# Kernel optimization log

Measured on AMD Instinct MI355X. Metric: run time of the kernel, lower is better.

## Reference

```python
import jax, jax.numpy as jnp
import numpy as np

BN_EPS = 1e-5
TAU = 1.0

def _conv(x, w, pad, groups=1):
    return jax.lax.conv_general_dilated(
        x, w, (1, 1), [(pad, pad), (pad, pad)],
        feature_group_count=groups,
        dimension_numbers=('NCHW', 'OIHW', 'NCHW'))

def _bn(x, p):
    # p: (4, C) rows = gamma, beta, running_mean, running_var (eval-mode BN)
    g, b, m, v = p[0], p[1], p[2], p[3]
    scale = g * jax.lax.rsqrt(v + BN_EPS)
    shift = b - m * scale
    return x * scale[None, :, None, None] + shift[None, :, None, None]

def _dsconv(x, dw, bn1, pw, bn2, pad):
    c = x.shape[1]
    h = jax.nn.silu(_bn(_conv(x, dw, pad, groups=c), bn1))
    return jax.nn.silu(_bn(_conv(h, pw, 0), bn2))

def _make_bn(key, ch):
    k1, k2, k3, k4 = jax.random.split(key, 4)
    g = 1.0 + 0.1 * jax.random.normal(k1, (ch,), jnp.float32)
    b = 0.1 * jax.random.normal(k2, (ch,), jnp.float32)
    m = 0.1 * jax.random.normal(k3, (ch,), jnp.float32)
    v = 0.5 + jax.random.uniform(k4, (ch,), jnp.float32)
    return jnp.stack([g, b, m, v])

def setup_inputs() -> dict:
    key = jax.random.key(0)
    ks = jax.random.split(key, 18)
    B, C, H, W = 4, 256, 128, 128
    P, K = 64, 8
    inp = {
        'x':      jax.random.normal(ks[0], (B, C, H, W), jnp.float32),
        'fp_w1':  0.05 * jax.random.normal(ks[1], (P, C, 1, 1), jnp.float32),
        'fp_bn1': _make_bn(ks[2], P),
        'fp_dw':  0.2 * jax.random.normal(ks[3], (P, 1, 3, 3), jnp.float32),
        'fp_bn2': _make_bn(ks[4], P),
        'protos': jax.random.normal(ks[5], (K, P), jnp.float32),
        'bs_dw':  0.2 * jax.random.normal(ks[6], (1, 1, 3, 3), jnp.float32),
        'bs_bn1': _make_bn(ks[7], 1),
        'bs_pw':  0.2 * jax.random.normal(ks[8], (8, 1, 1, 1), jnp.float32),
        'bs_bn2': _make_bn(ks[9], 8),
        'bl_dw':  0.2 * jax.random.normal(ks[10], (1, 1, 5, 5), jnp.float32),
        'bl_bn1': _make_bn(ks[11], 1),
        'bl_pw':  0.2 * jax.random.normal(ks[12], (8, 1, 1, 1), jnp.float32),
        'bl_bn2': _make_bn(ks[13], 8),
        'fuse_w': 0.2 * jax.random.normal(ks[14], (1, 16, 1, 1), jnp.float32),
        'fuse_b': 0.1 * jax.random.normal(ks[15], (1,), jnp.float32),
        'gamma':  0.5 * jax.random.normal(ks[16], (1,), jnp.float32),
    }
    return inp

def reference(x, fp_w1, fp_bn1, fp_dw, fp_bn2, protos,
              bs_dw, bs_bn1, bs_pw, bs_bn2,
              bl_dw, bl_bn1, bl_pw, bl_bn2,
              fuse_w, fuse_b, gamma):
    # feature_proj: 1x1 conv -> BN -> SiLU -> depthwise 3x3 -> BN -> SiLU
    h = jax.nn.silu(_bn(_conv(x, fp_w1, 0), fp_bn1))
    proj = jax.nn.silu(_bn(_conv(h, fp_dw, 1, groups=fp_dw.shape[0]), fp_bn2))

    # deviation: min L2 distance to K bg prototypes, per-image min-max normalized
    B, P, H, W = proj.shape
    feat = proj.reshape(B, P, H * W).transpose(0, 2, 1)      # (B, HW, P)
    d2 = ((feat * feat).sum(-1, keepdims=True)               # (B, HW, 1)
          + (protos * protos).sum(-1)                        # (K,)
          - 2.0 * jnp.einsum('bnp,kp->bnk', feat, protos))   # (B, HW, K)
    dist = jnp.sqrt(jnp.maximum(d2, 0.0))
    min_dist = dist.min(axis=2) / (TAU + 1e-6)               # (B, HW)
    d_min = min_dist.min(axis=1, keepdims=True)
    d_max = min_dist.max(axis=1, keepdims=True)
    deviation = ((min_dist - d_min) / (d_max - d_min + 1e-6)).reshape(B, 1, H, W)

    # deviation -> attention head: two DS-conv branches (3x3 and 5x5), fuse 1x1, sigmoid
    f1 = _dsconv(deviation, bs_dw, bs_bn1, bs_pw, bs_bn2, pad=1)
    f2 = _dsconv(deviation, bl_dw, bl_bn1, bl_pw, bl_bn2, pad=2)
    attn = jax.nn.sigmoid(_conv(jnp.concatenate([f1, f2], axis=1), fuse_w, 0)
                          + fuse_b[None, :, None, None])
    return x + gamma * (x * attn)
```

## Files before the change

### kernel.cpp

```cpp
#include <hip/hip_runtime.h>
#include <math.h>

#define C_IN 256
#define P_CH 64
#define H_IMG 128
#define W_IMG 128
#define HW (H_IMG*W_IMG)
#define N_IMG 4
#define K_PROTO 8
#define BN_EPS 1e-5f

#define OFF_WT     0
#define OFF_BIASA  16384
#define OFF_PNORM  16448
#define OFF_MINMAX 16456
#define OFF_H      16464
#define OFF_MD     (16464 + 4194304)
#define OFF_ATTN   (OFF_MD + 65536)

__device__ __forceinline__ float silu_f(float x) { return x / (1.f + __expf(-x)); }

__global__ void prep_kernel(const float* __restrict__ w1, const float* __restrict__ bn1,
                            const float* __restrict__ protos, float* __restrict__ ws)
{
    int bx = blockIdx.x, tid = threadIdx.x;
    if (bx < 64) {
        int idx = bx * 256 + tid;
        int c = idx >> 6, p = idx & 63;
        float sc = bn1[p] * rsqrtf(bn1[192 + p] + BN_EPS);
        ws[OFF_WT + idx] = w1[p * C_IN + c] * sc;
    } else {
        if (tid < 64) {
            float sc = bn1[tid] * rsqrtf(bn1[192 + tid] + BN_EPS);
            ws[OFF_BIASA + tid] = bn1[64 + tid] - bn1[128 + tid] * sc;
        }
        if (tid < 8) {
            float s = 0.f;
            for (int p = 0; p < 64; ++p) { float v = protos[tid * 64 + p]; s += v * v; }
            ws[OFF_PNORM + tid] = s;
        }
        if (tid < 4) {
            unsigned* mm = (unsigned*)(ws + OFF_MINMAX);
            mm[tid * 2]     = 0x7f7fffffu;
            mm[tid * 2 + 1] = 0u;
        }
    }
}

__global__ __launch_bounds__(256, 2) void conv1x1_kernel(
    const float* __restrict__ x, const float* __restrict__ wt,
    const float* __restrict__ bias, float* __restrict__ h)
{
    __shared__ float xs[2][8][128];
    int bx = blockIdx.x;
    int img = bx >> 7;
    int row = bx & 127;
    int tid = threadIdx.x;
    int pgrp = tid >> 6;
    int lane = tid & 63;
    int sc_ = tid >> 5;
    int sp_ = (tid & 31) * 4;

    const float* xbase = x + (size_t)img * C_IN * HW + row * W_IMG;
    float* hb = h + (size_t)img * P_CH * HW + row * W_IMG;

    float a0[16], a1[16];
#pragma unroll
    for (int j = 0; j < 16; ++j) { a0[j] = 0.f; a1[j] = 0.f; }

    {
        float4 f0 = *(const float4*)(xbase + (size_t)sc_ * HW + sp_);
        *(float4*)&xs[0][sc_][sp_] = f0;
    }
    __syncthreads();

    for (int k = 0; k < 32; ++k) {
        float4 nxt;
        if (k < 31)
            nxt = *(const float4*)(xbase + (size_t)((k + 1) * 8 + sc_) * HW + sp_);

        const float (*xb)[128] = xs[k & 1];
        int c0 = k * 8;
#pragma unroll
        for (int cl = 0; cl < 8; ++cl) {
            float xv0 = xb[cl][lane];
            float xv1 = xb[cl][lane + 64];
            int wof = __builtin_amdgcn_readfirstlane((c0 + cl) * 64 + pgrp * 16);
            const float* w = wt + wof;
#pragma unroll
            for (int j = 0; j < 16; ++j) {
                a0[j] = fmaf(xv0, w[j], a0[j]);
                a1[j] = fmaf(xv1, w[j], a1[j]);
            }
        }
        if (k < 31)
            *(float4*)&xs[(k + 1) & 1][sc_][sp_] = nxt;
        __syncthreads();
    }

    int bof = __builtin_amdgcn_readfirstlane(pgrp * 16);
#pragma unroll
    for (int j = 0; j < 16; ++j) {
        int p = bof + j;
        float bb = bias[p];
        hb[(size_t)p * HW + lane]      = silu_f(a0[j] + bb);
        hb[(size_t)p * HW + lane + 64] = silu_f(a1[j] + bb);
    }
}

__global__ __launch_bounds__(256) void dwconv_dev_kernel(
    const float* __restrict__ h, const float* __restrict__ dw,
    const float* __restrict__ bn2, const float* __restrict__ protos,
    const float* __restrict__ pnorm, float* __restrict__ md,
    unsigned* __restrict__ minmax)
{
    __shared__ float tile[2][8 * 324];
    __shared__ float red[512];
    int img = blockIdx.x >> 6;
    int t = blockIdx.x & 63;
    int y0 = (t >> 3) << 4, x0 = (t & 7) << 4;
    int tid = threadIdx.x;
    int ty = tid >> 4, tx = tid & 15;

    const float* himg = h + (size_t)img * P_CH * HW;

    int  pre_off[11];
    bool pre_ok[11];
    bool pre_v[11];
#pragma unroll
    for (int r = 0; r < 11; ++r) {
        int l = tid + r * 256;
        bool valid = l < 2592;
        int cl = l / 324;
        int rr = l - cl * 324;
        int ly = rr / 18, lx = rr - ly * 18;
        int yy = y0 - 1 + ly, xx = x0 - 1 + lx;
        bool inb = (yy >= 0) & (yy < H_IMG) & (xx >= 0) & (xx < W_IMG);
        pre_v[r] = valid;
        pre_ok[r] = valid && inb;
        pre_off[r] = cl * HW + (inb ? (yy * W_IMG + xx) : 0);
    }

    float norm2 = 0.f;
    float dot[K_PROTO];
#pragma unroll
    for (int k = 0; k < K_PROTO; ++k) dot[k] = 0.f;

    {
#pragma unroll
        for (int r = 0; r < 11; ++r) {
            float v = pre_ok[r] ? himg[pre_off[r]] : 0.f;
            if (pre_v[r]) tile[0][tid + r * 256] = v;
        }
    }
    __syncthreads();

    for (int k = 0; k < 8; ++k) {
        float pf[11];
        if (k < 7) {
            const float* hs = himg + (size_t)(k + 1) * 8 * HW;
#pragma unroll
            for (int r = 0; r < 11; ++r)
                pf[r] = pre_ok[r] ? hs[pre_off[r]] : 0.f;
        }

        const float* tb = tile[k & 1];
        int c0 = k * 8;
#pragma unroll
        for (int cl = 0; cl < 8; ++cl) {
            int ch = c0 + cl;
            const float* tc = tb + cl * 324;
            const float* wch = dw + ch * 9;
            float s = 0.f;
#pragma unroll
            for (int dy = 0; dy < 3; ++dy)
#pragma unroll
                for (int dx = 0; dx < 3; ++dx)
                    s = fmaf(tc[(ty + dy) * 18 + tx + dx], wch[dy * 3 + dx], s);
            float g = bn2[ch], bb = bn2[64 + ch], m = bn2[128 + ch], vv = bn2[192 + ch];
            float scale = g * rsqrtf(vv + BN_EPS);
            float val = silu_f(scale * s + (bb - m * scale));
            norm2 = fmaf(val, val, norm2);
#pragma unroll
            for (int kk = 0; kk < K_PROTO; ++kk)
                dot[kk] = fmaf(val, protos[kk * 64 + ch], dot[kk]);
        }

        if (k < 7) {
            float* tn = tile[(k + 1) & 1];
#pragma unroll
            for (int r = 0; r < 11; ++r)
                if (pre_v[r]) tn[tid + r * 256] = pf[r];
        }
        __syncthreads();
    }

    float d2min = 1e30f;
#pragma unroll
    for (int k = 0; k < K_PROTO; ++k)
        d2min = fminf(d2min, norm2 + pnorm[k] - 2.f * dot[k]);
    float mdv = sqrtf(fmaxf(d2min, 0.f)) * (1.f / 1.000001f);
    md[img * HW + (y0 + ty) * W_IMG + (x0 + tx)] = mdv;

    red[tid] = mdv; red[256 + tid] = mdv;
    __syncthreads();
    for (int s2 = 128; s2 > 0; s2 >>= 1) {
        if (tid < s2) {
            red[tid]       = fminf(red[tid], red[tid + s2]);
            red[256 + tid] = fmaxf(red[256 + tid], red[256 + tid + s2]);
        }
        __syncthreads();
    }
    if (tid == 0) {
        atomicMin(&minmax[img * 2],     __float_as_uint(red[0]));
        atomicMax(&minmax[img * 2 + 1], __float_as_uint(red[256]));
    }
}

__global__ __launch_bounds__(256) void attn_kernel(
    const float* __restrict__ md, const unsigned* __restrict__ minmax,
    const float* __restrict__ bs_dw, const float* __restrict__ bs_bn1,
    const float* __restrict__ bs_pw, const float* __restrict__ bs_bn2,
    const float* __restrict__ bl_dw, const float* __restrict__ bl_bn1,
    const float* __restrict__ bl_pw, const float* __restrict__ bl_bn2,
    const float* __restrict__ fuse_w, const float* __restrict__ fuse_b,
    float* __restrict__ attn)
{
    __shared__ float tile[20 * 20];
    int img = blockIdx.x >> 6;
    int t = blockIdx.x & 63;
    int y0 = (t >> 3) << 4, x0 = (t & 7) << 4;
    int tid = threadIdx.x;
    int ty = tid >> 4, tx = tid & 15;

    float fdmin = __uint_as_float(minmax[img * 2]);
    float fdmax = __uint_as_float(minmax[img * 2 + 1]);
    float inv = 1.f / (fdmax - fdmin + 1e-6f);

    const float* mdi = md + img * HW;
    for (int l = tid; l < 400; l += 256) {
        int ly = l / 20, lx = l - ly * 20;
        int yy = y0 - 2 + ly, xx = x0 - 2 + lx;
        float v = 0.f;
        if (yy >= 0 && yy < H_IMG && xx >= 0 && xx < W_IMG)
            v = (mdi[yy * W_IMG + xx] - fdmin) * inv;
        tile[l] = v;
    }
    __syncthreads();

    float c3 = 0.f;
#pragma unroll
    for (int dy = 0; dy < 3; ++dy)
#pragma unroll
        for (int dx = 0; dx < 3; ++dx)
            c3 = fmaf(tile[(ty + 1 + dy) * 20 + tx + 1 + dx], bs_dw[dy * 3 + dx], c3);
    float c5 = 0.f;
#pragma unroll
    for (int dy = 0; dy < 5; ++dy)
#pragma unroll
        for (int dx = 0; dx < 5; ++dx)
            c5 = fmaf(tile[(ty + dy) * 20 + tx + dx], bl_dw[dy * 5 + dx], c5);

    float s1 = bs_bn1[0] * rsqrtf(bs_bn1[3] + BN_EPS);
    float t1 = silu_f(s1 * c3 + (bs_bn1[1] - bs_bn1[2] * s1));
    float s2 = bl_bn1[0] * rsqrtf(bl_bn1[3] + BN_EPS);
    float t2 = silu_f(s2 * c5 + (bl_bn1[1] - bl_bn1[2] * s2));

    float acc = fuse_b[0];
#pragma unroll
    for (int c = 0; c < 8; ++c) {
        float scs = bs_bn2[c] * rsqrtf(bs_bn2[24 + c] + BN_EPS);
        float u1 = silu_f(scs * (bs_pw[c] * t1) + (bs_bn2[8 + c] - bs_bn2[16 + c] * scs));
        acc = fmaf(fuse_w[c], u1, acc);
        float scl = bl_bn2[c] * rsqrtf(bl_bn2[24 + c] + BN_EPS);
        float u2 = silu_f(scl * (bl_pw[c] * t2) + (bl_bn2[8 + c] - bl_bn2[16 + c] * scl));
        acc = fmaf(fuse_w[8 + c], u2, acc);
    }
    float a = 1.f / (1.f + __expf(-acc));
    attn[img * HW + (y0 + ty) * W_IMG + (x0 + tx)] = a;
}

__global__ __launch_bounds__(256) void final_kernel(
    const float* __restrict__ x, const float* __restrict__ attn,
    const float* __restrict__ gamma, float* __restrict__ out)
{
    size_t i = ((size_t)blockIdx.x * 256 + (size_t)threadIdx.x) * 4;
    float g = gamma[0];
    int b = (int)(i / ((size_t)C_IN * HW));
    int hw = (int)(i % HW);
    const float4 xv = *(const float4*)(x + i);
    const float4 av = *(const float4*)(attn + (size_t)b * HW + hw);
    float4 o;
    o.x = xv.x * (1.f + g * av.x);
    o.y = xv.y * (1.f + g * av.y);
    o.z = xv.z * (1.f + g * av.z);
    o.w = xv.w * (1.f + g * av.w);
    *(float4*)(out + i) = o;
}

extern "C" void kernel_launch(void* const* d_in, const int* in_sizes, int n_in,
                              void* d_out, int out_size, void* d_ws, size_t ws_size,
                              hipStream_t stream) {
    const float* x      = (const float*)d_in[0];
    const float* fp_w1  = (const float*)d_in[1];
    const float* fp_bn1 = (const float*)d_in[2];
    const float* fp_dw  = (const float*)d_in[3];
    const float* fp_bn2 = (const float*)d_in[4];
    const float* protos = (const float*)d_in[5];
    const float* bs_dw  = (const float*)d_in[6];
    const float* bs_bn1 = (const float*)d_in[7];
    const float* bs_pw  = (const float*)d_in[8];
    const float* bs_bn2 = (const float*)d_in[9];
    const float* bl_dw  = (const float*)d_in[10];
    const float* bl_bn1 = (const float*)d_in[11];
    const float* bl_pw  = (const float*)d_in[12];
    const float* bl_bn2 = (const float*)d_in[13];
    const float* fuse_w = (const float*)d_in[14];
    const float* fuse_b = (const float*)d_in[15];
    const float* gamma  = (const float*)d_in[16];
    float* ws  = (float*)d_ws;
    float* out = (float*)d_out;

    prep_kernel<<<65, 256, 0, stream>>>(fp_w1, fp_bn1, protos, ws);
    conv1x1_kernel<<<512, 256, 0, stream>>>(x, ws + OFF_WT, ws + OFF_BIASA, ws + OFF_H);
    dwconv_dev_kernel<<<256, 256, 0, stream>>>(ws + OFF_H, fp_dw, fp_bn2, protos,
                                               ws + OFF_PNORM, ws + OFF_MD,
                                               (unsigned*)(ws + OFF_MINMAX));
    attn_kernel<<<256, 256, 0, stream>>>(ws + OFF_MD, (const unsigned*)(ws + OFF_MINMAX),
                                         bs_dw, bs_bn1, bs_pw, bs_bn2,
                                         bl_dw, bl_bn1, bl_pw, bl_bn2,
                                         fuse_w, fuse_b, ws + OFF_ATTN);
    final_kernel<<<16384, 256, 0, stream>>>(x, ws + OFF_ATTN, gamma, out);
}
```

Baseline: 225.2 us.

## Split conv1x1 rows into halves and split dwconv channels across four thread groups

The 1x1 conv kernel now processes half-rows (64 pixels) per block, doubling the grid to 1024 blocks with fewer accumulators per thread and a higher occupancy bound. The depthwise/deviation kernel uses 1024-thread blocks where four 256-thread groups each handle 16 channels. Partial norms and dot products are combined through shared memory, and the min/max reduction now uses wavefront shuffles. The aim is more parallelism on a 256-CU GPU, where the old grids underfilled the device. The cost is re-reading weights per half-row and extra shared-memory reduction and syncs.

```diff
diff --git a/kernel.cpp b/kernel.cpp
--- a/kernel.cpp
+++ b/kernel.cpp
@@ -47,53 +47,50 @@
     }
 }
 
-__global__ __launch_bounds__(256, 2) void conv1x1_kernel(
+__global__ __launch_bounds__(256, 4) void conv1x1_kernel(
     const float* __restrict__ x, const float* __restrict__ wt,
     const float* __restrict__ bias, float* __restrict__ h)
 {
-    __shared__ float xs[2][8][128];
+    __shared__ float xs[2][8][64];
     int bx = blockIdx.x;
-    int img = bx >> 7;
-    int row = bx & 127;
+    int img = bx >> 8;
+    int rem = bx & 255;
+    int row = rem >> 1;
+    int half = rem & 1;
     int tid = threadIdx.x;
     int pgrp = tid >> 6;
     int lane = tid & 63;
-    int sc_ = tid >> 5;
-    int sp_ = (tid & 31) * 4;
-
-    const float* xbase = x + (size_t)img * C_IN * HW + row * W_IMG;
-    float* hb = h + (size_t)img * P_CH * HW + row * W_IMG;
-
-    float a0[16], a1[16];
-#pragma unroll
-    for (int j = 0; j < 16; ++j) { a0[j] = 0.f; a1[j] = 0.f; }
-
-    {
-        float4 f0 = *(const float4*)(xbase + (size_t)sc_ * HW + sp_);
-        *(float4*)&xs[0][sc_][sp_] = f0;
-    }
+    int sc_ = tid >> 4;
+    int sp_ = (tid & 15) * 4;
+
+    const float* xbase = x + (size_t)img * C_IN * HW + row * W_IMG + half * 64;
+    float* hb = h + (size_t)img * P_CH * HW + row * W_IMG + half * 64;
+
+    float acc[16];
+#pragma unroll
+    for (int j = 0; j < 16; ++j) acc[j] = 0.f;
+
+    if (tid < 128)
+        *(float4*)&xs[0][sc_][sp_] = *(const float4*)(xbase + (size_t)sc_ * HW + sp_);
     __syncthreads();
 
     for (int k = 0; k < 32; ++k) {
         float4 nxt;
-        if (k < 31)
+        if (k < 31 && tid < 128)
             nxt = *(const float4*)(xbase + (size_t)((k + 1) * 8 + sc_) * HW + sp_);
 
-        const float (*xb)[128] = xs[k & 1];
+        const float (*xb)[64] = xs[k & 1];
         int c0 = k * 8;
 #pragma unroll
         for (int cl = 0; cl < 8; ++cl) {
-            float xv0 = xb[cl][lane];
-            float xv1 = xb[cl][lane + 64];
+            float xv = xb[cl][lane];
             int wof = __builtin_amdgcn_readfirstlane((c0 + cl) * 64 + pgrp * 16);
             const float* w = wt + wof;
 #pragma unroll
-            for (int j = 0; j < 16; ++j) {
-                a0[j] = fmaf(xv0, w[j], a0[j]);
-                a1[j] = fmaf(xv1, w[j], a1[j]);
-            }
-        }
-        if (k < 31)
+            for (int j = 0; j < 16; ++j)
+                acc[j] = fmaf(xv, w[j], acc[j]);
+        }
+        if (k < 31 && tid < 128)
             *(float4*)&xs[(k + 1) & 1][sc_][sp_] = nxt;
         __syncthreads();
     }
@@ -102,34 +99,34 @@
 #pragma unroll
     for (int j = 0; j < 16; ++j) {
         int p = bof + j;
-        float bb = bias[p];
-        hb[(size_t)p * HW + lane]      = silu_f(a0[j] + bb);
-        hb[(size_t)p * HW + lane + 64] = silu_f(a1[j] + bb);
-    }
-}
-
-__global__ __launch_bounds__(256) void dwconv_dev_kernel(
+        hb[(size_t)p * HW + lane] = silu_f(acc[j] + bias[p]);
+    }
+}
+
+__global__ __launch_bounds__(1024) void dwconv_dev_kernel(
     const float* __restrict__ h, const float* __restrict__ dw,
     const float* __restrict__ bn2, const float* __restrict__ protos,
     const float* __restrict__ pnorm, float* __restrict__ md,
     unsigned* __restrict__ minmax)
 {
-    __shared__ float tile[2][8 * 324];
-    __shared__ float red[512];
+    __shared__ float smem[4 * 8 * 324];
     int img = blockIdx.x >> 6;
     int t = blockIdx.x & 63;
     int y0 = (t >> 3) << 4, x0 = (t & 7) << 4;
     int tid = threadIdx.x;
-    int ty = tid >> 4, tx = tid & 15;
+    int q = tid >> 8;
+    int qtid = tid & 255;
+    int ty = qtid >> 4, tx = qtid & 15;
 
     const float* himg = h + (size_t)img * P_CH * HW;
+    float* qt = smem + q * (8 * 324);
 
     int  pre_off[11];
     bool pre_ok[11];
     bool pre_v[11];
 #pragma unroll
     for (int r = 0; r < 11; ++r) {
-        int l = tid + r * 256;
+        int l = qtid + r * 256;
         bool valid = l < 2592;
         int cl = l / 324;
         int rr = l - cl * 324;
@@ -147,29 +144,29 @@
     for (int k = 0; k < K_PROTO; ++k) dot[k] = 0.f;
 
     {
+        const float* hs = himg + (size_t)(q * 16) * HW;
 #pragma unroll
         for (int r = 0; r < 11; ++r) {
-            float v = pre_ok[r] ? himg[pre_off[r]] : 0.f;
-            if (pre_v[r]) tile[0][tid + r * 256] = v;
-        }
-    }
-    __syncthreads();
-
-    for (int k = 0; k < 8; ++k) {
+            float v = pre_ok[r] ? hs[pre_off[r]] : 0.f;
+            if (pre_v[r]) qt[qtid + r * 256] = v;
+        }
+    }
+    __syncthreads();
+
+    for (int k = 0; k < 2; ++k) {
         float pf[11];
-        if (k < 7) {
-            const float* hs = himg + (size_t)(k + 1) * 8 * HW;
+        if (k == 0) {
+            const float* hs = himg + (size_t)(q * 16 + 8) * HW;
 #pragma unroll
             for (int r = 0; r < 11; ++r)
                 pf[r] = pre_ok[r] ? hs[pre_off[r]] : 0.f;
         }
 
-        const float* tb = tile[k & 1];
-        int c0 = k * 8;
+        int c0 = q * 16 + k * 8;
 #pragma unroll
         for (int cl = 0; cl < 8; ++cl) {
             int ch = c0 + cl;
-            const float* tc = tb + cl * 324;
+            const float* tc = qt + cl * 324;
             const float* wch = dw + ch * 9;
             float s = 0.f;
 #pragma unroll
@@ -186,34 +183,62 @@
                 dot[kk] = fmaf(val, protos[kk * 64 + ch], dot[kk]);
         }
 
-        if (k < 7) {
-            float* tn = tile[(k + 1) & 1];
+        if (k == 0) {
+            __syncthreads();
 #pragma unroll
             for (int r = 0; r < 11; ++r)
-                if (pre_v[r]) tn[tid + r * 256] = pf[r];
-        }
-        __syncthreads();
-    }
-
-    float d2min = 1e30f;
-#pragma unroll
-    for (int k = 0; k < K_PROTO; ++k)
-        d2min = fminf(d2min, norm2 + pnorm[k] - 2.f * dot[k]);
-    float mdv = sqrtf(fmaxf(d2min, 0.f)) * (1.f / 1.000001f);
-    md[img * HW + (y0 + ty) * W_IMG + (x0 + tx)] = mdv;
-
-    red[tid] = mdv; red[256 + tid] = mdv;
-    __syncthreads();
-    for (int s2 = 128; s2 > 0; s2 >>= 1) {
-        if (tid < s2) {
-            red[tid]       = fminf(red[tid], red[tid + s2]);
-            red[256 + tid] = fmaxf(red[256 + tid], red[256 + tid + s2]);
-        }
-        __syncthreads();
-    }
+                if (pre_v[r]) qt[qtid + r * 256] = pf[r];
+            __syncthreads();
+        }
+    }
+    __syncthreads();
+
+    float* P = smem;
+    {
+        float* dst = P + (q * 256 + qtid) * 9;
+        dst[0] = norm2;
+#pragma unroll
+        for (int kk = 0; kk < K_PROTO; ++kk) dst[1 + kk] = dot[kk];
+    }
+    __syncthreads();
+
+    float wmin = 1e30f, wmax = -1e30f, mdv = 0.f;
+    if (q == 0) {
+        float n2 = 0.f, dd[K_PROTO];
+#pragma unroll
+        for (int kk = 0; kk < K_PROTO; ++kk) dd[kk] = 0.f;
+#pragma unroll
+        for (int qq = 0; qq < 4; ++qq) {
+            const float* src = P + (qq * 256 + qtid) * 9;
+            n2 += src[0];
+#pragma unroll
+            for (int kk = 0; kk < K_PROTO; ++kk) dd[kk] += src[1 + kk];
+        }
+        float d2min = 1e30f;
+#pragma unroll
+        for (int kk = 0; kk < K_PROTO; ++kk)
+            d2min = fminf(d2min, n2 + pnorm[kk] - 2.f * dd[kk]);
+        mdv = sqrtf(fmaxf(d2min, 0.f)) * (1.f / 1.000001f);
+        md[img * HW + (y0 + ty) * W_IMG + (x0 + tx)] = mdv;
+        wmin = mdv; wmax = mdv;
+#pragma unroll
+        for (int d = 32; d > 0; d >>= 1) {
+            wmin = fminf(wmin, __shfl_xor(wmin, d));
+            wmax = fmaxf(wmax, __shfl_xor(wmax, d));
+        }
+    }
+    __syncthreads();
+    if (q == 0 && (qtid & 63) == 0) {
+        int wid = qtid >> 6;
+        smem[wid * 2]     = wmin;
+        smem[wid * 2 + 1] = wmax;
+    }
+    __syncthreads();
     if (tid == 0) {
-        atomicMin(&minmax[img * 2],     __float_as_uint(red[0]));
-        atomicMax(&minmax[img * 2 + 1], __float_as_uint(red[256]));
+        float bmin = fminf(fminf(smem[0], smem[2]), fminf(smem[4], smem[6]));
+        float bmax = fmaxf(fmaxf(smem[1], smem[3]), fmaxf(smem[5], smem[7]));
+        atomicMin(&minmax[img * 2],     __float_as_uint(bmin));
+        atomicMax(&minmax[img * 2 + 1], __float_as_uint(bmax));
     }
 }
 
@@ -322,10 +347,10 @@
     float* out = (float*)d_out;
 
     prep_kernel<<<65, 256, 0, stream>>>(fp_w1, fp_bn1, protos, ws);
-    conv1x1_kernel<<<512, 256, 0, stream>>>(x, ws + OFF_WT, ws + OFF_BIASA, ws + OFF_H);
-    dwconv_dev_kernel<<<256, 256, 0, stream>>>(ws + OFF_H, fp_dw, fp_bn2, protos,
-                                               ws + OFF_PNORM, ws + OFF_MD,
-                                               (unsigned*)(ws + OFF_MINMAX));
+    conv1x1_kernel<<<1024, 256, 0, stream>>>(x, ws + OFF_WT, ws + OFF_BIASA, ws + OFF_H);
+    dwconv_dev_kernel<<<256, 1024, 0, stream>>>(ws + OFF_H, fp_dw, fp_bn2, protos,
+                                                ws + OFF_PNORM, ws + OFF_MD,
+                                                (unsigned*)(ws + OFF_MINMAX));
     attn_kernel<<<256, 256, 0, stream>>>(ws + OFF_MD, (const unsigned*)(ws + OFF_MINMAX),
                                          bs_dw, bs_bn1, bs_pw, bs_bn2,
                                          bl_dw, bl_bn1, bl_pw, bl_bn2,
```

Measured after the change: 220.5 us. 2.1% less time.
